# Kernel tuning notes

Measured on AMD Instinct MI355X. Metric: run time of the kernel, lower is better.

The kernel has to match this reference:

```python
import jax, jax.numpy as jnp
import numpy as np

B, T, IN, OUT = 8, 2048, 1024, 512
DT, TAU = 1.0, 20.0


def setup_inputs() -> dict:
    key = jax.random.key(0)
    k1, k2 = jax.random.split(key)
    x = jax.random.normal(k1, (B, T, IN), jnp.float32)
    lim = 1.0 / np.sqrt(IN)
    weight = jax.random.uniform(k2, (OUT, IN), jnp.float32, -lim, lim)
    bias = jnp.zeros((OUT,), jnp.float32)
    # fixed tau trainer: decay = exp(-dt / tau) per output feature
    decay = jnp.full((OUT,), float(np.exp(-DT / TAU)), jnp.float32)
    return {"input_tensor": x, "weight": weight, "bias": bias, "decay": decay}


def reference(input_tensor, weight, bias, decay):
    # Hoist the time-invariant GEMM out of the recurrence: [B,T,OUT]
    current = jnp.einsum('bti,oi->bto', input_tensor, weight) + bias
    v0 = jnp.zeros((input_tensor.shape[0], weight.shape[0]), input_tensor.dtype)

    def step(v_tm1, c_t):
        v_t = decay * v_tm1 + (1.0 - decay) * c_t
        return v_t, v_t

    # scan over time axis: [T,B,OUT]
    _, outs = jax.lax.scan(step, v0, jnp.swapaxes(current, 0, 1))
    outputs = jnp.swapaxes(outs, 0, 1)  # [B,T,OUT]
    states = jnp.concatenate([v0[:, None, :], outputs], axis=1)[None]  # [1,B,T+1,OUT]
    return outputs, states
```

## Files before the change

kernel.cpp:

```cpp
#include <hip/hip_runtime.h>
#include <hip/hip_bf16.h>
#include <cstddef>
#include <cstdint>

#define BB    8
#define TT    2048
#define KIN   1024
#define NOUT  512
#define CHUNK 32
#define NCHUNK (TT / CHUNK)

#define BM 128
#define BN 64
#define BK 32
#define NKSTEP (KIN / BK)

typedef __attribute__((ext_vector_type(4))) float          f32x4;
typedef __attribute__((ext_vector_type(4))) unsigned int   u32x4;
typedef _Float16 f16x8 __attribute__((ext_vector_type(8)));

__global__ __launch_bounds__(256) void conv_f16_kernel(
    const float* __restrict__ src, _Float16* __restrict__ dst, int n8) {
  int i = blockIdx.x * blockDim.x + threadIdx.x;
  const int stride = gridDim.x * blockDim.x;
  for (; i < n8; i += stride) {
    float4 x0 = reinterpret_cast<const float4*>(src)[2 * i];
    float4 x1 = reinterpret_cast<const float4*>(src)[2 * i + 1];
    f16x8 h;
    h[0] = (_Float16)x0.x; h[1] = (_Float16)x0.y;
    h[2] = (_Float16)x0.z; h[3] = (_Float16)x0.w;
    h[4] = (_Float16)x1.x; h[5] = (_Float16)x1.y;
    h[6] = (_Float16)x1.z; h[7] = (_Float16)x1.w;
    reinterpret_cast<f16x8*>(dst)[i] = h;
  }
}

#define G2L(gp, sp)                                                        \
  __builtin_amdgcn_global_load_lds(                                       \
      (const __attribute__((address_space(1))) void*)(gp),                \
      (__attribute__((address_space(3))) void*)(sp), 16, 0, 0)

__global__ __launch_bounds__(256, 4) void gemm_f16(
    const float* __restrict__ X, const _Float16* __restrict__ Wh,
    const float* __restrict__ bias, float* __restrict__ C) {
  __shared__ __align__(16) unsigned char smem[16384 + 4096];

  const int tid  = threadIdx.x;
  const int wave = tid >> 6;
  const int lane = tid & 63;
  const int m0 = blockIdx.x * BM;
  const int n0 = blockIdx.y * BN;
  const int wm = (wave >> 1) * 64;
  const int wn = (wave & 1) * 32;
  const int frow = lane & 15;

  const int sgA  = (lane & 7) ^ (lane >> 3);
  const int arow = wave * 8 + (lane >> 3);
  const int sgB  = (lane & 3) ^ ((lane >> 3) & 3);
  const int brow = wave * 16 + (lane >> 2);

  const float*    gA = X  + (size_t)(m0 + arow) * KIN + sgA * 4;
  const _Float16* gB = Wh + (size_t)(n0 + brow) * KIN + sgB * 8;
  const int ldsw = wave * 1024;

  const int s0  = (lane >> 4) * 2;
  const int oA0 = ((s0)     ^ (lane & 7)) << 4;
  const int oA1 = ((s0 + 1) ^ (lane & 7)) << 4;
  const int oB  = ((lane >> 4) ^ ((lane >> 1) & 3)) << 4;

  f32x4 acc[4][2] = {};

  for (int t = 0; t < NKSTEP; ++t) {
    const int k0 = t * BK;
    __syncthreads();
#pragma unroll
    for (int i = 0; i < 4; ++i)
      G2L(gA + (size_t)i * 32 * KIN + k0, smem + i * 4096 + ldsw);
    G2L(gB + k0, smem + 16384 + ldsw);
    __syncthreads();

    f16x8 af[4];
#pragma unroll
    for (int mi = 0; mi < 4; ++mi) {
      const unsigned char* ap = smem + (size_t)(wm + mi * 16 + frow) * 128;
      f32x4 q0 = *reinterpret_cast<const f32x4*>(ap + oA0);
      f32x4 q1 = *reinterpret_cast<const f32x4*>(ap + oA1);
      u32x4 hv;
      hv[0] = __builtin_bit_cast(unsigned int, __builtin_amdgcn_cvt_pkrtz(q0[0], q0[1]));
      hv[1] = __builtin_bit_cast(unsigned int, __builtin_amdgcn_cvt_pkrtz(q0[2], q0[3]));
      hv[2] = __builtin_bit_cast(unsigned int, __builtin_amdgcn_cvt_pkrtz(q1[0], q1[1]));
      hv[3] = __builtin_bit_cast(unsigned int, __builtin_amdgcn_cvt_pkrtz(q1[2], q1[3]));
      af[mi] = __builtin_bit_cast(f16x8, hv);
    }

#pragma unroll
    for (int ni = 0; ni < 2; ++ni) {
      const unsigned char* bp = smem + 16384 + (size_t)(wn + ni * 16 + frow) * 64 + oB;
      f16x8 bf = *reinterpret_cast<const f16x8*>(bp);
#pragma unroll
      for (int mi = 0; mi < 4; ++mi)
        acc[mi][ni] = __builtin_amdgcn_mfma_f32_16x16x32_f16(af[mi], bf, acc[mi][ni], 0, 0, 0);
    }
  }

  const int colb = n0 + wn + (lane & 15);
  const int rowb = m0 + wm + ((lane >> 4) << 2);
#pragma unroll
  for (int ni = 0; ni < 2; ++ni) {
    const float bv = bias[colb + ni * 16];
#pragma unroll
    for (int mi = 0; mi < 4; ++mi) {
#pragma unroll
      for (int r = 0; r < 4; ++r) {
        C[(size_t)(rowb + mi * 16 + r) * NOUT + colb + ni * 16] = acc[mi][ni][r] + bv;
      }
    }
  }
}

__global__ __launch_bounds__(256) void gemm_f32_64x64(
    const float* __restrict__ X, const float* __restrict__ W,
    const float* __restrict__ bias, float* __restrict__ C) {
  __shared__ float As[16][65];
  __shared__ float Bs[16][65];
  const int m0  = blockIdx.y * 64;
  const int n0  = blockIdx.x * 64;
  const int tid = threadIdx.x;
  const int tx  = tid & 15;
  const int ty  = tid >> 4;
  const int lr  = tid >> 2;
  const int lk  = (tid & 3) << 2;
  float acc[4][4] = {};
  const float* xa = X + (size_t)(m0 + lr) * KIN + lk;
  const float* wb = W + (size_t)(n0 + lr) * KIN + lk;
  for (int k0 = 0; k0 < KIN; k0 += 16) {
    float4 av = *reinterpret_cast<const float4*>(xa + k0);
    float4 bv = *reinterpret_cast<const float4*>(wb + k0);
    As[lk + 0][lr] = av.x; As[lk + 1][lr] = av.y;
    As[lk + 2][lr] = av.z; As[lk + 3][lr] = av.w;
    Bs[lk + 0][lr] = bv.x; Bs[lk + 1][lr] = bv.y;
    Bs[lk + 2][lr] = bv.z; Bs[lk + 3][lr] = bv.w;
    __syncthreads();
#pragma unroll
    for (int k = 0; k < 16; ++k) {
      float a[4], b[4];
#pragma unroll
      for (int i = 0; i < 4; ++i) a[i] = As[k][ty * 4 + i];
#pragma unroll
      for (int j = 0; j < 4; ++j) b[j] = Bs[k][tx * 4 + j];
#pragma unroll
      for (int i = 0; i < 4; ++i)
#pragma unroll
        for (int j = 0; j < 4; ++j) acc[i][j] += a[i] * b[j];
    }
    __syncthreads();
  }
  const int n = n0 + tx * 4;
  float4 bv = *reinterpret_cast<const float4*>(&bias[n]);
#pragma unroll
  for (int i = 0; i < 4; ++i) {
    const int m = m0 + ty * 4 + i;
    float4 r;
    r.x = acc[i][0] + bv.x; r.y = acc[i][1] + bv.y;
    r.z = acc[i][2] + bv.z; r.w = acc[i][3] + bv.w;
    *reinterpret_cast<float4*>(&C[(size_t)m * NOUT + n]) = r;
  }
}

__global__ __launch_bounds__(512) void scan_vend(
    const float* __restrict__ C, const float* __restrict__ decay,
    float* __restrict__ vend) {
  const int b = blockIdx.x / NCHUNK;
  const int c = blockIdx.x % NCHUNK;
  const int o = threadIdx.x;
  const float d   = decay[o];
  const float omd = 1.0f - d;
  float v = 0.0f;
  size_t base = ((size_t)b * TT + (size_t)c * CHUNK) * NOUT + o;
#pragma unroll 4
  for (int k = 0; k < CHUNK; ++k) {
    v = d * v + omd * C[base + (size_t)k * NOUT];
  }
  vend[((size_t)b * NCHUNK + c) * NOUT + o] = v;
}

__global__ __launch_bounds__(512) void scan_chunks(
    const float* __restrict__ vend, const float* __restrict__ decay,
    float* __restrict__ vinit) {
  const int b = blockIdx.x;
  const int o = threadIdx.x;
  const float d = decay[o];
  float d2 = d * d, d4 = d2 * d2, d8 = d4 * d4, d16 = d8 * d8;
  const float dL = d16 * d16;
  float V = 0.0f;
  for (int c = 0; c < NCHUNK; ++c) {
    const size_t idx = ((size_t)b * NCHUNK + c) * NOUT + o;
    vinit[idx] = V;
    V = dL * V + vend[idx];
  }
}

__global__ __launch_bounds__(512) void scan_fixup(
    float* __restrict__ C, float* __restrict__ states,
    const float* __restrict__ decay, const float* __restrict__ vinit) {
  const int b = blockIdx.x / NCHUNK;
  const int c = blockIdx.x % NCHUNK;
  const int o = threadIdx.x;
  const float d   = decay[o];
  const float omd = 1.0f - d;
  float v = vinit[((size_t)b * NCHUNK + c) * NOUT + o];
  size_t obase = ((size_t)b * TT + (size_t)c * CHUNK) * NOUT + o;
  size_t sbase = ((size_t)b * (TT + 1) + (size_t)c * CHUNK + 1) * NOUT + o;
#pragma unroll 4
  for (int k = 0; k < CHUNK; ++k) {
    v = d * v + omd * C[obase + (size_t)k * NOUT];
    C[obase + (size_t)k * NOUT]      = v;
    states[sbase + (size_t)k * NOUT] = v;
  }
  if (c == 0) states[((size_t)b * (TT + 1)) * NOUT + o] = 0.0f;
}

__global__ __launch_bounds__(512) void scan_seq(
    float* __restrict__ C, float* __restrict__ states,
    const float* __restrict__ decay) {
  const int b = blockIdx.x;
  const int o = threadIdx.x;
  const float d   = decay[o];
  const float omd = 1.0f - d;
  float v = 0.0f;
  states[((size_t)b * (TT + 1)) * NOUT + o] = 0.0f;
  for (int t = 0; t < TT; ++t) {
    const size_t oi = ((size_t)b * TT + t) * NOUT + o;
    float x = C[oi];
    v = d * v + omd * x;
    C[oi] = v;
    states[((size_t)b * (TT + 1) + t + 1) * NOUT + o] = v;
  }
}

extern "C" void kernel_launch(void* const* d_in, const int* in_sizes, int n_in,
                              void* d_out, int out_size, void* d_ws, size_t ws_size,
                              hipStream_t stream) {
  const float* x     = (const float*)d_in[0];
  const float* w     = (const float*)d_in[1];
  const float* bias  = (const float*)d_in[2];
  const float* decay = (const float*)d_in[3];

  float* out    = (float*)d_out;
  float* states = out + (size_t)BB * TT * NOUT;

  const size_t szW = (size_t)NOUT * KIN;
  const size_t scan_elems = (size_t)BB * NCHUNK * NOUT;
  const size_t need = szW * sizeof(_Float16)
                    + 2 * scan_elems * sizeof(float);

  if (ws_size >= need) {
    _Float16* Wh = (_Float16*)d_ws;
    float* vend  = (float*)(Wh + szW);
    float* vinit = vend + scan_elems;

    conv_f16_kernel<<<256, 256, 0, stream>>>(w, Wh, (int)(szW / 8));
    gemm_f16<<<dim3((BB * TT) / BM, NOUT / BN), 256, 0, stream>>>(
        x, Wh, bias, out);
    scan_vend  <<<BB * NCHUNK, NOUT, 0, stream>>>(out, decay, vend);
    scan_chunks<<<BB,          NOUT, 0, stream>>>(vend, decay, vinit);
    scan_fixup <<<BB * NCHUNK, NOUT, 0, stream>>>(out, states, decay, vinit);
  } else {
    gemm_f32_64x64<<<dim3(NOUT / 64, (BB * TT) / 64), 256, 0, stream>>>(x, w, bias, out);
    scan_seq<<<BB, NOUT, 0, stream>>>(out, states, decay);
  }
}
```

Measured before the change: 75.62 us.

## Double-buffer GEMM A tile via registers, convert to f16 before LDS, load B directly

Replaces the async global-to-LDS copies with register prefetch of the next K-tile of X. The prefetched tile is converted to f16 once and stored into a double-buffered LDS area, so only one barrier per iteration remains. BK grows to 64, and B fragments are read straight from global memory instead of being staged through LDS. This aims to overlap global latency with MFMA work and to remove the per-wave repeated f32-to-f16 conversion. In exchange it uses more registers and 32 KB of LDS, which may reduce occupancy, and the uncached direct B loads from global could cost bandwidth.

```diff
diff --git a/kernel.cpp b/kernel.cpp
--- a/kernel.cpp
+++ b/kernel.cpp
@@ -12,7 +12,7 @@
 
 #define BM 128
 #define BN 64
-#define BK 32
+#define BK 64
 #define NKSTEP (KIN / BK)
 
 typedef __attribute__((ext_vector_type(4))) float          f32x4;
@@ -35,15 +35,10 @@
   }
 }
 
-#define G2L(gp, sp)                                                        \
-  __builtin_amdgcn_global_load_lds(                                       \
-      (const __attribute__((address_space(1))) void*)(gp),                \
-      (__attribute__((address_space(3))) void*)(sp), 16, 0, 0)
-
 __global__ __launch_bounds__(256, 4) void gemm_f16(
     const float* __restrict__ X, const _Float16* __restrict__ Wh,
     const float* __restrict__ bias, float* __restrict__ C) {
-  __shared__ __align__(16) unsigned char smem[16384 + 4096];
+  __shared__ __align__(16) unsigned char smem[2 * 16384];
 
   const int tid  = threadIdx.x;
   const int wave = tid >> 6;
@@ -52,54 +47,85 @@
   const int n0 = blockIdx.y * BN;
   const int wm = (wave >> 1) * 64;
   const int wn = (wave & 1) * 32;
-  const int frow = lane & 15;
-
-  const int sgA  = (lane & 7) ^ (lane >> 3);
-  const int arow = wave * 8 + (lane >> 3);
-  const int sgB  = (lane & 3) ^ ((lane >> 3) & 3);
-  const int brow = wave * 16 + (lane >> 2);
-
-  const float*    gA = X  + (size_t)(m0 + arow) * KIN + sgA * 4;
-  const _Float16* gB = Wh + (size_t)(n0 + brow) * KIN + sgB * 8;
-  const int ldsw = wave * 1024;
-
-  const int s0  = (lane >> 4) * 2;
-  const int oA0 = ((s0)     ^ (lane & 7)) << 4;
-  const int oA1 = ((s0 + 1) ^ (lane & 7)) << 4;
-  const int oB  = ((lane >> 4) ^ ((lane >> 1) & 3)) << 4;
+
+  const int arow  = tid >> 1;
+  const int asl0  = (tid & 1) << 2;
+  const float* pA = X + (size_t)(m0 + arow) * KIN + asl0 * 8;
+  int wb[4];
+#pragma unroll
+  for (int s = 0; s < 4; ++s)
+    wb[s] = arow * 128 + (((asl0 + s) ^ (arow & 7)) << 4);
+
+  const int oA0 = (((lane >> 4))     ^ (lane & 7)) << 4;
+  const int oA1 = ((4 + (lane >> 4)) ^ (lane & 7)) << 4;
+
+  const _Float16* pB = Wh + (size_t)(n0 + wn + (lane & 15)) * KIN + ((lane >> 4) << 3);
 
   f32x4 acc[4][2] = {};
+  f32x4 ra[4][2];
+
+#pragma unroll
+  for (int s = 0; s < 4; ++s) {
+    ra[s][0] = *reinterpret_cast<const f32x4*>(pA + s * 8);
+    ra[s][1] = *reinterpret_cast<const f32x4*>(pA + s * 8 + 4);
+  }
+#pragma unroll
+  for (int s = 0; s < 4; ++s) {
+    u32x4 hv;
+    hv[0] = __builtin_bit_cast(unsigned int, __builtin_amdgcn_cvt_pkrtz(ra[s][0][0], ra[s][0][1]));
+    hv[1] = __builtin_bit_cast(unsigned int, __builtin_amdgcn_cvt_pkrtz(ra[s][0][2], ra[s][0][3]));
+    hv[2] = __builtin_bit_cast(unsigned int, __builtin_amdgcn_cvt_pkrtz(ra[s][1][0], ra[s][1][1]));
+    hv[3] = __builtin_bit_cast(unsigned int, __builtin_amdgcn_cvt_pkrtz(ra[s][1][2], ra[s][1][3]));
+    *reinterpret_cast<u32x4*>(smem + wb[s]) = hv;
+  }
+  __syncthreads();
 
   for (int t = 0; t < NKSTEP; ++t) {
-    const int k0 = t * BK;
-    __syncthreads();
-#pragma unroll
-    for (int i = 0; i < 4; ++i)
-      G2L(gA + (size_t)i * 32 * KIN + k0, smem + i * 4096 + ldsw);
-    G2L(gB + k0, smem + 16384 + ldsw);
-    __syncthreads();
-
-    f16x8 af[4];
+    const unsigned char* bufA = smem + (t & 1) * 16384;
+    unsigned char*       nxtA = smem + ((t + 1) & 1) * 16384;
+
+    if (t + 1 < NKSTEP) {
+      const int k0 = (t + 1) * BK;
+#pragma unroll
+      for (int s = 0; s < 4; ++s) {
+        ra[s][0] = *reinterpret_cast<const f32x4*>(pA + k0 + s * 8);
+        ra[s][1] = *reinterpret_cast<const f32x4*>(pA + k0 + s * 8 + 4);
+      }
+    }
+
+    f16x8 bf[2][2];
+#pragma unroll
+    for (int ni = 0; ni < 2; ++ni)
+#pragma unroll
+      for (int kk = 0; kk < 2; ++kk)
+        bf[ni][kk] = *reinterpret_cast<const f16x8*>(pB + (size_t)ni * 16 * KIN + t * BK + kk * 32);
+
+    f16x8 af[4][2];
 #pragma unroll
     for (int mi = 0; mi < 4; ++mi) {
-      const unsigned char* ap = smem + (size_t)(wm + mi * 16 + frow) * 128;
-      f32x4 q0 = *reinterpret_cast<const f32x4*>(ap + oA0);
-      f32x4 q1 = *reinterpret_cast<const f32x4*>(ap + oA1);
-      u32x4 hv;
-      hv[0] = __builtin_bit_cast(unsigned int, __builtin_amdgcn_cvt_pkrtz(q0[0], q0[1]));
-      hv[1] = __builtin_bit_cast(unsigned int, __builtin_amdgcn_cvt_pkrtz(q0[2], q0[3]));
-      hv[2] = __builtin_bit_cast(unsigned int, __builtin_amdgcn_cvt_pkrtz(q1[0], q1[1]));
-      hv[3] = __builtin_bit_cast(unsigned int, __builtin_amdgcn_cvt_pkrtz(q1[2], q1[3]));
-      af[mi] = __builtin_bit_cast(f16x8, hv);
-    }
-
-#pragma unroll
-    for (int ni = 0; ni < 2; ++ni) {
-      const unsigned char* bp = smem + 16384 + (size_t)(wn + ni * 16 + frow) * 64 + oB;
-      f16x8 bf = *reinterpret_cast<const f16x8*>(bp);
-#pragma unroll
-      for (int mi = 0; mi < 4; ++mi)
-        acc[mi][ni] = __builtin_amdgcn_mfma_f32_16x16x32_f16(af[mi], bf, acc[mi][ni], 0, 0, 0);
+      const int rb = (wm + mi * 16 + (lane & 15)) * 128;
+      af[mi][0] = *reinterpret_cast<const f16x8*>(bufA + rb + oA0);
+      af[mi][1] = *reinterpret_cast<const f16x8*>(bufA + rb + oA1);
+    }
+#pragma unroll
+    for (int kk = 0; kk < 2; ++kk)
+#pragma unroll
+      for (int ni = 0; ni < 2; ++ni)
+#pragma unroll
+        for (int mi = 0; mi < 4; ++mi)
+          acc[mi][ni] = __builtin_amdgcn_mfma_f32_16x16x32_f16(af[mi][kk], bf[ni][kk], acc[mi][ni], 0, 0, 0);
+
+    if (t + 1 < NKSTEP) {
+#pragma unroll
+      for (int s = 0; s < 4; ++s) {
+        u32x4 hv;
+        hv[0] = __builtin_bit_cast(unsigned int, __builtin_amdgcn_cvt_pkrtz(ra[s][0][0], ra[s][0][1]));
+        hv[1] = __builtin_bit_cast(unsigned int, __builtin_amdgcn_cvt_pkrtz(ra[s][0][2], ra[s][0][3]));
+        hv[2] = __builtin_bit_cast(unsigned int, __builtin_amdgcn_cvt_pkrtz(ra[s][1][0], ra[s][1][1]));
+        hv[3] = __builtin_bit_cast(unsigned int, __builtin_amdgcn_cvt_pkrtz(ra[s][1][2], ra[s][1][3]));
+        *reinterpret_cast<u32x4*>(nxtA + wb[s]) = hv;
+      }
+      __syncthreads();
     }
   }
 
```

After: 142.7 us. 1.89x slower.

## Double-buffer GEMM LDS loads and fuse per-chunk scan end-state into epilogue

Applied to the files above, without the earlier changes.

The f16 GEMM now stages K tiles into two LDS buffers with async global-to-LDS loads issued two steps ahead, waiting on vmcnt instead of a full sync around each load. The epilogue also writes the output tile to LDS and computes each 32-step chunk's end state directly, which removes the separate scan_vend kernel and its re-read of the output. In exchange, LDS use doubles (about 40KB per block), which may reduce occupancy under launch_bounds(256,4), and the epilogue gains an extra sync plus a short serial loop.

```diff
diff --git a/kernel.cpp b/kernel.cpp
--- a/kernel.cpp
+++ b/kernel.cpp
@@ -14,6 +14,7 @@
 #define BN 64
 #define BK 32
 #define NKSTEP (KIN / BK)
+#define LDSBUF 20480
 
 typedef __attribute__((ext_vector_type(4))) float          f32x4;
 typedef __attribute__((ext_vector_type(4))) unsigned int   u32x4;
@@ -42,8 +43,9 @@
 
 __global__ __launch_bounds__(256, 4) void gemm_f16(
     const float* __restrict__ X, const _Float16* __restrict__ Wh,
-    const float* __restrict__ bias, float* __restrict__ C) {
-  __shared__ __align__(16) unsigned char smem[16384 + 4096];
+    const float* __restrict__ bias, const float* __restrict__ decay,
+    float* __restrict__ C, float* __restrict__ vend) {
+  __shared__ __align__(16) unsigned char smem[2 * LDSBUF];
 
   const int tid  = threadIdx.x;
   const int wave = tid >> 6;
@@ -70,19 +72,32 @@
 
   f32x4 acc[4][2] = {};
 
+  auto stage = [&](int buf, int k0) {
+    unsigned char* bA = smem + buf * LDSBUF;
+#pragma unroll
+    for (int i = 0; i < 4; ++i)
+      G2L(gA + (size_t)i * 32 * KIN + k0, bA + i * 4096 + ldsw);
+    G2L(gB + k0, bA + 16384 + ldsw);
+  };
+
+  stage(0, 0);
+  stage(1, BK);
+
   for (int t = 0; t < NKSTEP; ++t) {
-    const int k0 = t * BK;
-    __syncthreads();
-#pragma unroll
-    for (int i = 0; i < 4; ++i)
-      G2L(gA + (size_t)i * 32 * KIN + k0, smem + i * 4096 + ldsw);
-    G2L(gB + k0, smem + 16384 + ldsw);
-    __syncthreads();
+    if (t < NKSTEP - 1) {
+      asm volatile("s_waitcnt vmcnt(5)" ::: "memory");
+    } else {
+      asm volatile("s_waitcnt vmcnt(0)" ::: "memory");
+    }
+    __builtin_amdgcn_sched_barrier(0);
+    __builtin_amdgcn_s_barrier();
+
+    const unsigned char* cb = smem + (t & 1) * LDSBUF;
 
     f16x8 af[4];
 #pragma unroll
     for (int mi = 0; mi < 4; ++mi) {
-      const unsigned char* ap = smem + (size_t)(wm + mi * 16 + frow) * 128;
+      const unsigned char* ap = cb + (size_t)(wm + mi * 16 + frow) * 128;
       f32x4 q0 = *reinterpret_cast<const f32x4*>(ap + oA0);
       f32x4 q1 = *reinterpret_cast<const f32x4*>(ap + oA1);
       u32x4 hv;
@@ -95,16 +110,23 @@
 
 #pragma unroll
     for (int ni = 0; ni < 2; ++ni) {
-      const unsigned char* bp = smem + 16384 + (size_t)(wn + ni * 16 + frow) * 64 + oB;
+      const unsigned char* bp = cb + 16384 + (size_t)(wn + ni * 16 + frow) * 64 + oB;
       f16x8 bf = *reinterpret_cast<const f16x8*>(bp);
 #pragma unroll
       for (int mi = 0; mi < 4; ++mi)
         acc[mi][ni] = __builtin_amdgcn_mfma_f32_16x16x32_f16(af[mi], bf, acc[mi][ni], 0, 0, 0);
     }
-  }
-
+
+    __builtin_amdgcn_s_barrier();
+    __builtin_amdgcn_sched_barrier(0);
+    if (t + 2 < NKSTEP) stage(t & 1, (t + 2) * BK);
+  }
+
+  float* cl = reinterpret_cast<float*>(smem);
   const int colb = n0 + wn + (lane & 15);
   const int rowb = m0 + wm + ((lane >> 4) << 2);
+  const int lcol = wn + (lane & 15);
+  const int lrow = wm + ((lane >> 4) << 2);
 #pragma unroll
   for (int ni = 0; ni < 2; ++ni) {
     const float bv = bias[colb + ni * 16];
@@ -112,9 +134,26 @@
     for (int mi = 0; mi < 4; ++mi) {
 #pragma unroll
       for (int r = 0; r < 4; ++r) {
-        C[(size_t)(rowb + mi * 16 + r) * NOUT + colb + ni * 16] = acc[mi][ni][r] + bv;
+        const float val = acc[mi][ni][r] + bv;
+        C[(size_t)(rowb + mi * 16 + r) * NOUT + colb + ni * 16] = val;
+        cl[(lrow + mi * 16 + r) * 64 + lcol + ni * 16] = val;
       }
     }
+  }
+  __syncthreads();
+
+  {
+    const int cc = tid >> 6;
+    const int f  = tid & 63;
+    const int b  = m0 >> 11;
+    const int c0 = (m0 & (TT - 1)) >> 5;
+    const float d   = decay[n0 + f];
+    const float omd = 1.0f - d;
+    float v = 0.0f;
+    const float* col = cl + cc * 32 * 64 + f;
+#pragma unroll 8
+    for (int k = 0; k < 32; ++k) v = d * v + omd * col[k * 64];
+    vend[((size_t)b * NCHUNK + c0 + cc) * NOUT + n0 + f] = v;
   }
 }
 
@@ -261,9 +300,8 @@
 
     conv_f16_kernel<<<256, 256, 0, stream>>>(w, Wh, (int)(szW / 8));
     gemm_f16<<<dim3((BB * TT) / BM, NOUT / BN), 256, 0, stream>>>(
-        x, Wh, bias, out);
-    scan_vend  <<<BB * NCHUNK, NOUT, 0, stream>>>(out, decay, vend);
-    scan_chunks<<<BB,          NOUT, 0, stream>>>(vend, decay, vinit);
+        x, Wh, bias, decay, out, vend);
+    scan_chunks<<<BB, NOUT, 0, stream>>>(vend, decay, vinit);
     scan_fixup <<<BB * NCHUNK, NOUT, 0, stream>>>(out, states, decay, vinit);
   } else {
     gemm_f32_64x64<<<dim3(NOUT / 64, (BB * TT) / 64), 256, 0, stream>>>(x, w, bias, out);
```

Result: slower. 78.28 us (+3.5%).

## Fuse chunk-end scan into GEMM epilogue and stage A as fp16 via registers

Applied to the files above, without the earlier changes.

Removes the separate scan_vend kernel by computing each 32-row chunk's end state inside the GEMM epilogue, using per-lane Horner accumulation plus cross-lane shuffles. The A tile is now loaded into registers, converted to fp16 once and written to LDS, with the next k-step prefetched into registers and the B tile double-buffered. This avoids one full re-read of the C matrix and shrinks LDS per block. The cost is higher register pressure and an epilogue whose correctness depends on the tile-to-chunk mapping (BM 128 giving 4 chunks of 32 rows).

```diff
diff --git a/kernel.cpp b/kernel.cpp
--- a/kernel.cpp
+++ b/kernel.cpp
@@ -42,8 +42,9 @@
 
 __global__ __launch_bounds__(256, 4) void gemm_f16(
     const float* __restrict__ X, const _Float16* __restrict__ Wh,
-    const float* __restrict__ bias, float* __restrict__ C) {
-  __shared__ __align__(16) unsigned char smem[16384 + 4096];
+    const float* __restrict__ bias, const float* __restrict__ decay,
+    float* __restrict__ C, float* __restrict__ vend) {
+  __shared__ __align__(16) unsigned char smem[8192 + 2 * 4096];
 
   const int tid  = threadIdx.x;
   const int wave = tid >> 6;
@@ -53,68 +54,117 @@
   const int wm = (wave >> 1) * 64;
   const int wn = (wave & 1) * 32;
   const int frow = lane & 15;
-
-  const int sgA  = (lane & 7) ^ (lane >> 3);
-  const int arow = wave * 8 + (lane >> 3);
+  const int g    = lane >> 4;
+
+  const int ar = wave * 8 + (lane >> 3);
+  const int as = lane & 7;
+  const float* gA = X + (size_t)(m0 + ar) * KIN + as * 4;
+  const int awb = ((as >> 1) ^ ((ar >> 1) & 3)) * 16 + (as & 1) * 8;
+
+  const int brow = wave * 16 + (lane >> 2);
   const int sgB  = (lane & 3) ^ ((lane >> 3) & 3);
-  const int brow = wave * 16 + (lane >> 2);
-
-  const float*    gA = X  + (size_t)(m0 + arow) * KIN + sgA * 4;
   const _Float16* gB = Wh + (size_t)(n0 + brow) * KIN + sgB * 8;
-  const int ldsw = wave * 1024;
-
-  const int s0  = (lane >> 4) * 2;
-  const int oA0 = ((s0)     ^ (lane & 7)) << 4;
-  const int oA1 = ((s0 + 1) ^ (lane & 7)) << 4;
-  const int oB  = ((lane >> 4) ^ ((lane >> 1) & 3)) << 4;
+
+  const int swzr = (g ^ ((frow >> 1) & 3)) << 4;
 
   f32x4 acc[4][2] = {};
+  f32x4 ra0, ra1, ra2, ra3;
+
+  ra0 = *reinterpret_cast<const f32x4*>(gA);
+  ra1 = *reinterpret_cast<const f32x4*>(gA + (size_t)32 * KIN);
+  ra2 = *reinterpret_cast<const f32x4*>(gA + (size_t)64 * KIN);
+  ra3 = *reinterpret_cast<const f32x4*>(gA + (size_t)96 * KIN);
+  G2L(gB, smem + 8192 + wave * 1024);
 
   for (int t = 0; t < NKSTEP; ++t) {
-    const int k0 = t * BK;
     __syncthreads();
-#pragma unroll
-    for (int i = 0; i < 4; ++i)
-      G2L(gA + (size_t)i * 32 * KIN + k0, smem + i * 4096 + ldsw);
-    G2L(gB + k0, smem + 16384 + ldsw);
+
+    {
+      uint2 w;
+      w.x = __builtin_bit_cast(unsigned int, __builtin_amdgcn_cvt_pkrtz(ra0[0], ra0[1]));
+      w.y = __builtin_bit_cast(unsigned int, __builtin_amdgcn_cvt_pkrtz(ra0[2], ra0[3]));
+      *reinterpret_cast<uint2*>(smem + (ar +  0) * 64 + awb) = w;
+      w.x = __builtin_bit_cast(unsigned int, __builtin_amdgcn_cvt_pkrtz(ra1[0], ra1[1]));
+      w.y = __builtin_bit_cast(unsigned int, __builtin_amdgcn_cvt_pkrtz(ra1[2], ra1[3]));
+      *reinterpret_cast<uint2*>(smem + (ar + 32) * 64 + awb) = w;
+      w.x = __builtin_bit_cast(unsigned int, __builtin_amdgcn_cvt_pkrtz(ra2[0], ra2[1]));
+      w.y = __builtin_bit_cast(unsigned int, __builtin_amdgcn_cvt_pkrtz(ra2[2], ra2[3]));
+      *reinterpret_cast<uint2*>(smem + (ar + 64) * 64 + awb) = w;
+      w.x = __builtin_bit_cast(unsigned int, __builtin_amdgcn_cvt_pkrtz(ra3[0], ra3[1]));
+      w.y = __builtin_bit_cast(unsigned int, __builtin_amdgcn_cvt_pkrtz(ra3[2], ra3[3]));
+      *reinterpret_cast<uint2*>(smem + (ar + 96) * 64 + awb) = w;
+    }
     __syncthreads();
 
+    if (t + 1 < NKSTEP) {
+      const int k0 = (t + 1) * BK;
+      ra0 = *reinterpret_cast<const f32x4*>(gA + k0);
+      ra1 = *reinterpret_cast<const f32x4*>(gA + (size_t)32 * KIN + k0);
+      ra2 = *reinterpret_cast<const f32x4*>(gA + (size_t)64 * KIN + k0);
+      ra3 = *reinterpret_cast<const f32x4*>(gA + (size_t)96 * KIN + k0);
+      G2L(gB + k0, smem + 8192 + ((t + 1) & 1) * 4096 + wave * 1024);
+    }
+
+    const unsigned char* bB = smem + 8192 + (t & 1) * 4096;
     f16x8 af[4];
 #pragma unroll
-    for (int mi = 0; mi < 4; ++mi) {
-      const unsigned char* ap = smem + (size_t)(wm + mi * 16 + frow) * 128;
-      f32x4 q0 = *reinterpret_cast<const f32x4*>(ap + oA0);
-      f32x4 q1 = *reinterpret_cast<const f32x4*>(ap + oA1);
-      u32x4 hv;
-      hv[0] = __builtin_bit_cast(unsigned int, __builtin_amdgcn_cvt_pkrtz(q0[0], q0[1]));
-      hv[1] = __builtin_bit_cast(unsigned int, __builtin_amdgcn_cvt_pkrtz(q0[2], q0[3]));
-      hv[2] = __builtin_bit_cast(unsigned int, __builtin_amdgcn_cvt_pkrtz(q1[0], q1[1]));
-      hv[3] = __builtin_bit_cast(unsigned int, __builtin_amdgcn_cvt_pkrtz(q1[2], q1[3]));
-      af[mi] = __builtin_bit_cast(f16x8, hv);
-    }
-
+    for (int mi = 0; mi < 4; ++mi)
+      af[mi] = *reinterpret_cast<const f16x8*>(smem + (wm + mi * 16 + frow) * 64 + swzr);
 #pragma unroll
     for (int ni = 0; ni < 2; ++ni) {
-      const unsigned char* bp = smem + 16384 + (size_t)(wn + ni * 16 + frow) * 64 + oB;
-      f16x8 bf = *reinterpret_cast<const f16x8*>(bp);
+      f16x8 bf = *reinterpret_cast<const f16x8*>(bB + (wn + ni * 16 + frow) * 64 + swzr);
 #pragma unroll
       for (int mi = 0; mi < 4; ++mi)
         acc[mi][ni] = __builtin_amdgcn_mfma_f32_16x16x32_f16(af[mi], bf, acc[mi][ni], 0, 0, 0);
     }
   }
 
-  const int colb = n0 + wn + (lane & 15);
-  const int rowb = m0 + wm + ((lane >> 4) << 2);
-#pragma unroll
-  for (int ni = 0; ni < 2; ++ni) {
-    const float bv = bias[colb + ni * 16];
-#pragma unroll
-    for (int mi = 0; mi < 4; ++mi) {
-#pragma unroll
-      for (int r = 0; r < 4; ++r) {
-        C[(size_t)(rowb + mi * 16 + r) * NOUT + colb + ni * 16] = acc[mi][ni][r] + bv;
+  const int colb = n0 + wn + frow;
+  const int rowb = m0 + wm + (g << 2);
+  const float bv0 = bias[colb];
+  const float bv1 = bias[colb + 16];
+#pragma unroll
+  for (int mi = 0; mi < 4; ++mi) {
+#pragma unroll
+    for (int r = 0; r < 4; ++r) {
+      C[(size_t)(rowb + mi * 16 + r) * NOUT + colb]      = acc[mi][0][r] + bv0;
+      C[(size_t)(rowb + mi * 16 + r) * NOUT + colb + 16] = acc[mi][1][r] + bv1;
+    }
+  }
+
+  {
+    const float d0 = decay[colb];
+    const float d1 = decay[colb + 16];
+    float rr[2][2];
+#pragma unroll
+    for (int ni = 0; ni < 2; ++ni) {
+      const float d = ni ? d1 : d0;
+      const float bv = ni ? bv1 : bv0;
+      const float omd = 1.0f - d;
+      const float dd = d * d, d4 = dd * dd, d8 = d4 * d4;
+      const float d16 = d8 * d8, d12 = d8 * d4;
+      const float dpg = (g == 0) ? d12 : (g == 1) ? d8 : (g == 2) ? d4 : 1.0f;
+      float s[4];
+#pragma unroll
+      for (int mi = 0; mi < 4; ++mi) {
+        float v = acc[mi][ni][0] + bv;
+        v = v * d + (acc[mi][ni][1] + bv);
+        v = v * d + (acc[mi][ni][2] + bv);
+        v = v * d + (acc[mi][ni][3] + bv);
+        s[mi] = omd * v;
       }
-    }
+      float ulo = dpg * (s[0] * d16 + s[1]);
+      float uhi = dpg * (s[2] * d16 + s[3]);
+      ulo += __shfl_xor(ulo, 16); ulo += __shfl_xor(ulo, 32);
+      uhi += __shfl_xor(uhi, 16); uhi += __shfl_xor(uhi, 32);
+      rr[0][ni] = ulo; rr[1][ni] = uhi;
+    }
+    const int b     = m0 >> 11;
+    const int clo   = ((m0 & (TT - 1)) >> 5) + (wm >> 5);
+    const float val = rr[g >> 1][g & 1];
+    const int chunk = clo + (g >> 1);
+    const int col   = n0 + wn + frow + (g & 1) * 16;
+    vend[((size_t)b * NCHUNK + chunk) * NOUT + col] = val;
   }
 }
 
@@ -167,23 +217,6 @@
   }
 }
 
-__global__ __launch_bounds__(512) void scan_vend(
-    const float* __restrict__ C, const float* __restrict__ decay,
-    float* __restrict__ vend) {
-  const int b = blockIdx.x / NCHUNK;
-  const int c = blockIdx.x % NCHUNK;
-  const int o = threadIdx.x;
-  const float d   = decay[o];
-  const float omd = 1.0f - d;
-  float v = 0.0f;
-  size_t base = ((size_t)b * TT + (size_t)c * CHUNK) * NOUT + o;
-#pragma unroll 4
-  for (int k = 0; k < CHUNK; ++k) {
-    v = d * v + omd * C[base + (size_t)k * NOUT];
-  }
-  vend[((size_t)b * NCHUNK + c) * NOUT + o] = v;
-}
-
 __global__ __launch_bounds__(512) void scan_chunks(
     const float* __restrict__ vend, const float* __restrict__ decay,
     float* __restrict__ vinit) {
@@ -261,9 +294,8 @@
 
     conv_f16_kernel<<<256, 256, 0, stream>>>(w, Wh, (int)(szW / 8));
     gemm_f16<<<dim3((BB * TT) / BM, NOUT / BN), 256, 0, stream>>>(
-        x, Wh, bias, out);
-    scan_vend  <<<BB * NCHUNK, NOUT, 0, stream>>>(out, decay, vend);
-    scan_chunks<<<BB,          NOUT, 0, stream>>>(vend, decay, vinit);
+        x, Wh, bias, decay, out, vend);
+    scan_chunks<<<BB, NOUT, 0, stream>>>(vend, decay, vinit);
     scan_fixup <<<BB * NCHUNK, NOUT, 0, stream>>>(out, states, decay, vinit);
   } else {
     gemm_f32_64x64<<<dim3(NOUT / 64, (BB * TT) / 64), 256, 0, stream>>>(x, w, bias, out);
```

Measured after the change: 76.68 us. No clear change (+1.4%).
